# Performance work log

Measured on AMD Instinct MI355X. Metric: run time of the kernel, lower is better.

Reference implementation:

```python
import jax, jax.numpy as jnp
import numpy as np

N, C, H, W = 8, 256, 31, 31
HIDDEN, OUT = 512, 256


def setup_inputs() -> dict:
    key = jax.random.key(0)
    k0, k1, k2, k3, k4 = jax.random.split(key, 5)
    x = jax.random.normal(k0, (N, C, H, W), dtype=jnp.float32)
    # Linear params (torch nn.Linear layout: [out_features, in_features])
    W1 = jax.random.normal(k1, (HIDDEN, C), dtype=jnp.float32) * (1.0 / np.sqrt(C))
    b1 = jax.random.normal(k2, (HIDDEN,), dtype=jnp.float32) * 0.01
    W2 = jax.random.normal(k3, (OUT, HIDDEN), dtype=jnp.float32) * (1.0 / np.sqrt(HIDDEN))
    b2 = jax.random.normal(k4, (OUT,), dtype=jnp.float32) * 0.01
    return {"x": x, "W1": W1, "b1": b1, "W2": W2, "b2": b2}


def _normalized_adjacency(n, h, w):
    M = n * h * w
    idx = jnp.arange(M)
    blk = idx // (h * w)          # sample id of each node
    pos = idx % (h * w)           # spatial position within sample
    # block-diagonal all-ones per sample
    same_block = (blk[:, None] == blk[None, :]).astype(jnp.float32)
    # identity link between consecutive samples (disjoint from block-diag)
    neighbor = ((jnp.abs(blk[:, None] - blk[None, :]) == 1)
                & (pos[:, None] == pos[None, :])).astype(jnp.float32)
    A = same_block + neighbor + jnp.eye(M, dtype=jnp.float32)
    deg = A.sum(axis=1)
    dinv = jnp.where(deg > 0, deg ** -0.5, 0.0)
    return A * dinv[:, None] * dinv[None, :]  # D^-1/2 A D^-1/2


def reference(x, W1, b1, W2, b2):
    n, c, h, w = x.shape
    weight = _normalized_adjacency(n, h, w)                 # [M, M]
    nodes = x.transpose(0, 2, 3, 1).reshape(-1, c)          # [M, C]
    hid = jax.nn.leaky_relu(weight @ nodes @ W1.T + b1)     # [M, HIDDEN]
    hid = jax.nn.leaky_relu(weight @ hid @ W2.T + b2)       # [M, OUT]
    hid = hid.reshape(n, h, w, -1).transpose(0, 3, 1, 2)    # [N, OUT, H, W]
    return hid.max(axis=0, keepdims=True)                   # [1, OUT, H, W]
```

## Files before the change

### kernel.cpp

```cpp
#include <hip/hip_runtime.h>
#include <math.h>

#define NS   8
#define CC   256
#define PP   961
#define MM   7688
#define MP   7744
#define HID  512
#define OUTC 256

typedef _Float16 h16;
using half8   = __attribute__((ext_vector_type(8))) _Float16;
using floatx4 = __attribute__((ext_vector_type(4))) float;

#define AS1 __attribute__((address_space(1)))
#define AS3 __attribute__((address_space(3)))

__device__ __forceinline__ float dinv_of(int b) {
    return (b == 0 || b == NS - 1) ? 0.0322245515f : 0.0322078318f;
}

__global__ void prep(const float* __restrict__ W1, const float* __restrict__ W2,
                     h16* __restrict__ w1h, h16* __restrict__ w2h,
                     const float* __restrict__ x, h16* __restrict__ Xt,
                     float* __restrict__ S1p, float* __restrict__ SY) {
    int blk = blockIdx.x, tid = threadIdx.x;
    if (blk < 256) {
        bool second = blk >= 128;
        const float* src = second ? W2 : W1;
        h16* dst = second ? w2h : w1h;
        int i = ((blk & 127) * 256 + tid) * 4;
        float4 v = *(const float4*)(src + i);
        dst[i + 0] = (h16)v.x; dst[i + 1] = (h16)v.y;
        dst[i + 2] = (h16)v.z; dst[i + 3] = (h16)v.w;
    } else if (blk < 2240) {
        __shared__ h16 tr[32][33];
        int t = blk - 256;
        int b = t & 7, ct = (t >> 3) & 7, pt = t >> 6;
        int p0 = pt * 32, c0 = ct * 32;
        int j = tid & 31, i0 = tid >> 5;
        int p = p0 + j;
        #pragma unroll
        for (int r = 0; r < 4; ++r) {
            int c = c0 + i0 + r * 8;
            float v = (p < PP) ? x[((size_t)b * CC + c) * PP + p] : 0.f;
            tr[i0 + r * 8][j] = (h16)v;
        }
        __syncthreads();
        #pragma unroll
        for (int r = 0; r < 4; ++r) {
            int ii = tid & 31;
            int jj = (tid >> 5) + r * 8;
            int pw = p0 + jj;
            if (pw < PP) {
                int row = ((pw >> 3) << 6) + (b << 3) + (pw & 7);
                Xt[(size_t)row * CC + c0 + ii] = tr[ii][jj];
            }
        }
        if (tid < 32) {
            float s = 0.f;
            #pragma unroll
            for (int jj = 0; jj < 32; ++jj) s += (float)tr[tid][jj];
            S1p[pt * (NS * CC) + b * CC + c0 + tid] = s;
        }
    } else {
        for (int i = tid; i < NS * OUTC; i += 256) SY[i] = 0.f;
    }
}

__global__ void corr(const float* __restrict__ S1p, const float* __restrict__ W1,
                     float* __restrict__ SZc) {
    __shared__ float s1[CC];
    int b = blockIdx.x >> 2, hq = blockIdx.x & 3;
    int tid = threadIdx.x;
    if (tid < CC) {
        float s = 0.f;
        for (int pt = 0; pt < 31; ++pt) s += S1p[pt * (NS * CC) + b * CC + tid];
        s1[tid] = s;
    }
    __syncthreads();
    if (tid < 128) {
        int h = hq * 128 + tid;
        const float* wr = W1 + (size_t)h * CC;
        float dot = 0.f;
        for (int c = 0; c < CC; c += 4) {
            float4 w = *(const float4*)(wr + c);
            dot += s1[c] * w.x + s1[c + 1] * w.y + s1[c + 2] * w.z + s1[c + 3] * w.w;
        }
        float db = dinv_of(b);
        SZc[b * HID + h] = db * db * dot;
    }
}

__global__ __launch_bounds__(256) void gemm1_rho(
    const h16* __restrict__ Xt,
    const h16* __restrict__ B,
    const float* __restrict__ SZc,
    const float* __restrict__ b1v,
    h16* __restrict__ H1)
{
    __shared__ __align__(16) h16 Xs[64 * 64];
    __shared__ __align__(16) h16 Gs[64 * 64];
    __shared__ __align__(16) h16 Bs[64 * 64];
    int tid = threadIdx.x, wave = tid >> 6, lane = tid & 63;
    int rt = blockIdx.x, n0 = blockIdx.y * 64;
    int sro = lane >> 3;
    int sch = (lane & 7) ^ sro;
    const h16* gx0 = Xt + (size_t)(rt * 64 + wave * 16 + sro) * CC + sch * 8;
    const h16* gb0 = B + (size_t)(n0 + wave * 16 + sro) * CC + sch * 8;
    h16* lx0 = &Xs[(wave * 16) * 64];
    h16* lx1 = &Xs[(wave * 16 + 8) * 64];
    h16* lb0 = &Bs[(wave * 16) * 64];
    h16* lb1 = &Bs[(wave * 16 + 8) * 64];
    int fr = lane & 15, fq = lane >> 4;
    int hr = tid >> 2, hc0 = (tid & 3) * 2;
    int hb = hr >> 3;
    float db  = dinv_of(hb);
    float db2 = db * db;
    float dmw = (hb > 0)      ? db * dinv_of(hb - 1) : 0.f;
    float dpw = (hb < NS - 1) ? db * dinv_of(hb + 1) : 0.f;
    int hrm = (hb > 0)      ? hr - 8 : hr;
    int hrp = (hb < NS - 1) ? hr + 8 : hr;
    floatx4 acc[4] = {{0.f,0.f,0.f,0.f},{0.f,0.f,0.f,0.f},{0.f,0.f,0.f,0.f},{0.f,0.f,0.f,0.f}};
    for (int kk = 0; kk < CC; kk += 64) {
        __builtin_amdgcn_global_load_lds((const AS1 void*)(const void*)(gx0 + kk),
                                         (AS3 void*)(void*)lx0, 16, 0, 0);
        __builtin_amdgcn_global_load_lds((const AS1 void*)(const void*)(gx0 + 8 * CC + kk),
                                         (AS3 void*)(void*)lx1, 16, 0, 0);
        __builtin_amdgcn_global_load_lds((const AS1 void*)(const void*)(gb0 + kk),
                                         (AS3 void*)(void*)lb0, 16, 0, 0);
        __builtin_amdgcn_global_load_lds((const AS1 void*)(const void*)(gb0 + 8 * CC + kk),
                                         (AS3 void*)(void*)lb1, 16, 0, 0);
        __syncthreads();
        #pragma unroll
        for (int qi = 0; qi < 2; ++qi) {
            int ch = hc0 + qi;
            int slot = ch ^ (hr & 7);
            half8 zc = *(const half8*)&Xs[hr  * 64 + slot * 8];
            half8 zm = *(const half8*)&Xs[hrm * 64 + slot * 8];
            half8 zp = *(const half8*)&Xs[hrp * 64 + slot * 8];
            half8 o;
            #pragma unroll
            for (int j = 0; j < 8; ++j)
                o[j] = (h16)(db2 * (float)zc[j] + dmw * (float)zm[j] + dpw * (float)zp[j]);
            *(half8*)&Gs[hr * 64 + slot * 8] = o;
        }
        __syncthreads();
        #pragma unroll
        for (int ks = 0; ks < 2; ++ks) {
            int slot = (ks * 4 + fq) ^ (fr & 7);
            half8 bf = *(const half8*)&Bs[(wave * 16 + fr) * 64 + slot * 8];
            #pragma unroll
            for (int mb = 0; mb < 4; ++mb) {
                half8 af = *(const half8*)&Gs[(mb * 16 + fr) * 64 + slot * 8];
                acc[mb] = __builtin_amdgcn_mfma_f32_16x16x32_f16(af, bf, acc[mb], 0, 0, 0);
            }
        }
        __syncthreads();
    }
    int col = n0 + wave * 16 + fr;
    float bv = b1v[col];
    #pragma unroll
    for (int mb = 0; mb < 4; ++mb) {
        #pragma unroll
        for (int r = 0; r < 4; ++r) {
            int row = 16 * mb + 4 * fq + r;
            int b = row >> 3;
            int p = rt * 8 + (row & 7);
            float v = acc[mb][r] + SZc[b * HID + col] + bv;
            v = (v >= 0.f) ? v : 0.01f * v;
            H1[(size_t)(rt * 64 + row) * HID + col] = (p < PP) ? (h16)v : (h16)0.f;
        }
    }
}

__global__ __launch_bounds__(256) void gemm2_sy(
    const h16* __restrict__ A,
    const h16* __restrict__ B,
    float* __restrict__ Y,
    float* __restrict__ SY)
{
    __shared__ __align__(16) h16 As[64 * 64];
    __shared__ __align__(16) h16 Bs[64 * 64];
    int tid = threadIdx.x, wave = tid >> 6, lane = tid & 63;
    int rt = blockIdx.x, n0 = blockIdx.y * 64;
    int sro = lane >> 3;
    int sch = (lane & 7) ^ sro;
    const h16* ga0 = A + (size_t)(rt * 64 + wave * 16 + sro) * HID + sch * 8;
    const h16* gb0 = B + (size_t)(n0 + wave * 16 + sro) * HID + sch * 8;
    h16* la0 = &As[(wave * 16) * 64];
    h16* la1 = &As[(wave * 16 + 8) * 64];
    h16* lb0 = &Bs[(wave * 16) * 64];
    h16* lb1 = &Bs[(wave * 16 + 8) * 64];
    int fr = lane & 15, fq = lane >> 4;
    floatx4 acc[4] = {{0.f,0.f,0.f,0.f},{0.f,0.f,0.f,0.f},{0.f,0.f,0.f,0.f},{0.f,0.f,0.f,0.f}};
    for (int kk = 0; kk < HID; kk += 64) {
        __builtin_amdgcn_global_load_lds((const AS1 void*)(const void*)(ga0 + kk),
                                         (AS3 void*)(void*)la0, 16, 0, 0);
        __builtin_amdgcn_global_load_lds((const AS1 void*)(const void*)(ga0 + 8 * HID + kk),
                                         (AS3 void*)(void*)la1, 16, 0, 0);
        __builtin_amdgcn_global_load_lds((const AS1 void*)(const void*)(gb0 + kk),
                                         (AS3 void*)(void*)lb0, 16, 0, 0);
        __builtin_amdgcn_global_load_lds((const AS1 void*)(const void*)(gb0 + 8 * HID + kk),
                                         (AS3 void*)(void*)lb1, 16, 0, 0);
        __syncthreads();
        #pragma unroll
        for (int ks = 0; ks < 2; ++ks) {
            int slot = (ks * 4 + fq) ^ (fr & 7);
            half8 bf = *(const half8*)&Bs[(wave * 16 + fr) * 64 + slot * 8];
            #pragma unroll
            for (int mb = 0; mb < 4; ++mb) {
                half8 af = *(const half8*)&As[(mb * 16 + fr) * 64 + slot * 8];
                acc[mb] = __builtin_amdgcn_mfma_f32_16x16x32_f16(af, bf, acc[mb], 0, 0, 0);
            }
        }
        __syncthreads();
    }
    int col = n0 + wave * 16 + fr;
    size_t row0 = (size_t)rt * 64;
    float sb[4];
    #pragma unroll
    for (int mb = 0; mb < 4; ++mb) {
        float s = 0.f;
        #pragma unroll
        for (int r = 0; r < 4; ++r) {
            int row = 16 * mb + 4 * fq + r;
            float v = acc[mb][r];
            Y[(row0 + row) * OUTC + col] = v;
            s += v;
        }
        sb[mb] = s;
    }
    #pragma unroll
    for (int mb = 0; mb < 4; ++mb) sb[mb] += __shfl_xor(sb[mb], 16);
    if (fq == 0 || fq == 2) {
        int bodd = (fq >= 2) ? 1 : 0;
        #pragma unroll
        for (int mb = 0; mb < 4; ++mb)
            atomicAdd(&SY[(2 * mb + bodd) * OUTC + col], sb[mb]);
    }
}

__global__ void final_max(const float* __restrict__ Y, const float* __restrict__ SY,
                          const float* __restrict__ b2, float* __restrict__ out) {
    int pt = blockIdx.x, ot = blockIdx.y;
    int p0 = pt * 32, o0 = ot * 32;
    __shared__ float t[32][33];
    int i = threadIdx.x & 31, j0 = threadIdx.x >> 5;
    int o = o0 + i;
    float bias = b2[o];
    #pragma unroll
    for (int r = 0; r < 4; ++r) {
        int j = j0 + r * 8;
        int p = p0 + j;
        float vmax = -INFINITY;
        if (p < PP) {
            size_t rbase = (size_t)(((p >> 3) << 6) + (p & 7)) * OUTC + o;
            float y[NS];
            #pragma unroll
            for (int b = 0; b < NS; ++b)
                y[b] = Y[rbase + (size_t)b * 8 * OUTC];
            #pragma unroll
            for (int b = 0; b < NS; ++b) {
                float db = dinv_of(b);
                float a = db * (SY[b * OUTC + o] + y[b]);
                if (b > 0)      a += dinv_of(b - 1) * y[b - 1];
                if (b < NS - 1) a += dinv_of(b + 1) * y[b + 1];
                float z = db * a + bias;
                z = (z >= 0.f) ? z : 0.01f * z;
                vmax = fmaxf(vmax, z);
            }
        }
        t[j][i] = vmax;
    }
    __syncthreads();
    int jj = threadIdx.x & 31, ii0 = threadIdx.x >> 5;
    #pragma unroll
    for (int r = 0; r < 4; ++r) {
        int ii = ii0 + r * 8;
        int pw = p0 + jj;
        if (pw < PP)
            out[(size_t)(o0 + ii) * PP + pw] = t[jj][ii];
    }
}

extern "C" void kernel_launch(void* const* d_in, const int* in_sizes, int n_in,
                              void* d_out, int out_size, void* d_ws, size_t ws_size,
                              hipStream_t stream) {
    const float* x  = (const float*)d_in[0];
    const float* W1 = (const float*)d_in[1];
    const float* b1 = (const float*)d_in[2];
    const float* W2 = (const float*)d_in[3];
    const float* b2 = (const float*)d_in[4];
    float* out = (float*)d_out;
    float* ws  = (float*)d_ws;

    float* S1p = ws;
    float* SZc = ws + 63488;
    float* SY  = ws + 67584;
    h16*  w1h  = (h16*)(ws + 69632);
    h16*  w2h  = (h16*)(ws + 135168);
    h16*  Xt   = (h16*)(ws + 200704);
    h16*  H1   = (h16*)(ws + 1191936);
    float* Y   = ws + 3174400;

    prep<<<2241, 256, 0, stream>>>(W1, W2, w1h, w2h, x, Xt, S1p, SY);
    corr<<<32, 256, 0, stream>>>(S1p, W1, SZc);
    gemm1_rho<<<dim3(MP / 64, HID / 64), 256, 0, stream>>>(Xt, w1h, SZc, b1, H1);
    gemm2_sy<<<dim3(MP / 64, OUTC / 64), 256, 0, stream>>>(H1, w2h, Y, SY);
    final_max<<<dim3(31, 8), 256, 0, stream>>>(Y, SY, b2, out);
}
```

Measured before the change: 103.5 us.

## Move neighbor mixing into prep and fold per-sample correction rows into gemm1

The inter-sample neighbor mixing (rho) now happens once in prep, written directly as fp16 G, instead of being recomputed per column tile inside gemm1. The per-sample block-sum correction becomes extra rows appended to G, so gemm1 computes it as an extra row tile and the separate corr kernel disappears. The correction add, bias and leaky-relu move into gemm2's A-operand load, which uses register loads instead of direct-to-LDS loads. This removes one launch and the redundant LDS mixing work, but gemm2's A path now pays for extra global loads and ALU work per tile.

New measurement: 99.31 us. 4.1% less time.

```diff
diff --git a/kernel.cpp b/kernel.cpp
--- a/kernel.cpp
+++ b/kernel.cpp
@@ -6,6 +6,7 @@
 #define PP   961
 #define MM   7688
 #define MP   7744
+#define MPX  7808
 #define HID  512
 #define OUTC 256
 
@@ -22,159 +23,135 @@
 
 __global__ void prep(const float* __restrict__ W1, const float* __restrict__ W2,
                      h16* __restrict__ w1h, h16* __restrict__ w2h,
-                     const float* __restrict__ x, h16* __restrict__ Xt,
-                     float* __restrict__ S1p, float* __restrict__ SY) {
+                     const float* __restrict__ x, h16* __restrict__ G,
+                     float* __restrict__ SY) {
     int blk = blockIdx.x, tid = threadIdx.x;
-    if (blk < 256) {
-        bool second = blk >= 128;
+    if (blk < 248) {
+        __shared__ float tr[8][32][33];
+        int pt = blk % 31, ct = blk / 31;
+        int p0 = pt * 32, c0 = ct * 32;
+        int j = tid & 31, i0 = tid >> 5;
+        int p = p0 + j;
+        bool pv = (p < PP);
+        #pragma unroll
+        for (int b = 0; b < NS; ++b)
+            #pragma unroll
+            for (int r = 0; r < 4; ++r) {
+                int c = c0 + i0 + r * 8;
+                tr[b][i0 + r * 8][j] = pv ? x[((size_t)b * CC + c) * PP + p] : 0.f;
+            }
+        __syncthreads();
+        int ii = tid & 31, jj0 = tid >> 5;
+        #pragma unroll
+        for (int b = 0; b < NS; ++b) {
+            float db  = dinv_of(b);
+            float db2 = db * db;
+            float dmw = (b > 0)      ? db * dinv_of(b - 1) : 0.f;
+            float dpw = (b < NS - 1) ? db * dinv_of(b + 1) : 0.f;
+            #pragma unroll
+            for (int r = 0; r < 4; ++r) {
+                int pj = jj0 + r * 8;
+                int pw = p0 + pj;
+                if (pw < 968) {
+                    float v = 0.f;
+                    if (pw < PP) {
+                        v = db2 * tr[b][ii][pj];
+                        if (b > 0)      v += dmw * tr[b - 1][ii][pj];
+                        if (b < NS - 1) v += dpw * tr[b + 1][ii][pj];
+                    }
+                    int row = ((pw >> 3) << 6) + (b << 3) + (pw & 7);
+                    G[(size_t)row * CC + c0 + ii] = (h16)v;
+                }
+            }
+        }
+    } else if (blk < 2296) {
+        int t = blk - 248;
+        int b = t >> 8, c = t & 255;
+        const float* src = x + ((size_t)b * CC + c) * PP;
+        float s = 0.f;
+        for (int i = tid; i < PP; i += 256) s += src[i];
+        __shared__ float red[256];
+        red[tid] = s;
+        __syncthreads();
+        for (int off = 128; off > 0; off >>= 1) {
+            if (tid < off) red[tid] += red[tid + off];
+            __syncthreads();
+        }
+        if (tid == 0) {
+            float db = dinv_of(b);
+            G[(size_t)(MP + b) * CC + c] = (h16)(db * db * red[0]);
+        }
+    } else if (blk < 2552) {
+        int t = blk - 2296;
+        bool second = t >= 128;
         const float* src = second ? W2 : W1;
         h16* dst = second ? w2h : w1h;
-        int i = ((blk & 127) * 256 + tid) * 4;
+        int i = ((t & 127) * 256 + tid) * 4;
         float4 v = *(const float4*)(src + i);
         dst[i + 0] = (h16)v.x; dst[i + 1] = (h16)v.y;
         dst[i + 2] = (h16)v.z; dst[i + 3] = (h16)v.w;
-    } else if (blk < 2240) {
-        __shared__ h16 tr[32][33];
-        int t = blk - 256;
-        int b = t & 7, ct = (t >> 3) & 7, pt = t >> 6;
-        int p0 = pt * 32, c0 = ct * 32;
-        int j = tid & 31, i0 = tid >> 5;
-        int p = p0 + j;
-        #pragma unroll
-        for (int r = 0; r < 4; ++r) {
-            int c = c0 + i0 + r * 8;
-            float v = (p < PP) ? x[((size_t)b * CC + c) * PP + p] : 0.f;
-            tr[i0 + r * 8][j] = (h16)v;
-        }
-        __syncthreads();
-        #pragma unroll
-        for (int r = 0; r < 4; ++r) {
-            int ii = tid & 31;
-            int jj = (tid >> 5) + r * 8;
-            int pw = p0 + jj;
-            if (pw < PP) {
-                int row = ((pw >> 3) << 6) + (b << 3) + (pw & 7);
-                Xt[(size_t)row * CC + c0 + ii] = tr[ii][jj];
-            }
-        }
-        if (tid < 32) {
-            float s = 0.f;
-            #pragma unroll
-            for (int jj = 0; jj < 32; ++jj) s += (float)tr[tid][jj];
-            S1p[pt * (NS * CC) + b * CC + c0 + tid] = s;
-        }
     } else {
         for (int i = tid; i < NS * OUTC; i += 256) SY[i] = 0.f;
-    }
-}
-
-__global__ void corr(const float* __restrict__ S1p, const float* __restrict__ W1,
-                     float* __restrict__ SZc) {
-    __shared__ float s1[CC];
-    int b = blockIdx.x >> 2, hq = blockIdx.x & 3;
-    int tid = threadIdx.x;
-    if (tid < CC) {
-        float s = 0.f;
-        for (int pt = 0; pt < 31; ++pt) s += S1p[pt * (NS * CC) + b * CC + tid];
-        s1[tid] = s;
-    }
-    __syncthreads();
-    if (tid < 128) {
-        int h = hq * 128 + tid;
-        const float* wr = W1 + (size_t)h * CC;
-        float dot = 0.f;
-        for (int c = 0; c < CC; c += 4) {
-            float4 w = *(const float4*)(wr + c);
-            dot += s1[c] * w.x + s1[c + 1] * w.y + s1[c + 2] * w.z + s1[c + 3] * w.w;
-        }
-        float db = dinv_of(b);
-        SZc[b * HID + h] = db * db * dot;
-    }
-}
-
-__global__ __launch_bounds__(256) void gemm1_rho(
-    const h16* __restrict__ Xt,
+        for (int i = tid; i < 56 * CC; i += 256)
+            G[(size_t)(MP + NS) * CC + i] = (h16)0.f;
+    }
+}
+
+__global__ __launch_bounds__(256) void gemm1(
+    const h16* __restrict__ A,
     const h16* __restrict__ B,
-    const float* __restrict__ SZc,
     const float* __restrict__ b1v,
     h16* __restrict__ H1)
 {
-    __shared__ __align__(16) h16 Xs[64 * 64];
-    __shared__ __align__(16) h16 Gs[64 * 64];
+    __shared__ __align__(16) h16 As[64 * 64];
     __shared__ __align__(16) h16 Bs[64 * 64];
     int tid = threadIdx.x, wave = tid >> 6, lane = tid & 63;
     int rt = blockIdx.x, n0 = blockIdx.y * 64;
     int sro = lane >> 3;
     int sch = (lane & 7) ^ sro;
-    const h16* gx0 = Xt + (size_t)(rt * 64 + wave * 16 + sro) * CC + sch * 8;
+    const h16* ga0 = A + (size_t)(rt * 64 + wave * 16 + sro) * CC + sch * 8;
     const h16* gb0 = B + (size_t)(n0 + wave * 16 + sro) * CC + sch * 8;
-    h16* lx0 = &Xs[(wave * 16) * 64];
-    h16* lx1 = &Xs[(wave * 16 + 8) * 64];
+    h16* la0 = &As[(wave * 16) * 64];
+    h16* la1 = &As[(wave * 16 + 8) * 64];
     h16* lb0 = &Bs[(wave * 16) * 64];
     h16* lb1 = &Bs[(wave * 16 + 8) * 64];
     int fr = lane & 15, fq = lane >> 4;
-    int hr = tid >> 2, hc0 = (tid & 3) * 2;
-    int hb = hr >> 3;
-    float db  = dinv_of(hb);
-    float db2 = db * db;
-    float dmw = (hb > 0)      ? db * dinv_of(hb - 1) : 0.f;
-    float dpw = (hb < NS - 1) ? db * dinv_of(hb + 1) : 0.f;
-    int hrm = (hb > 0)      ? hr - 8 : hr;
-    int hrp = (hb < NS - 1) ? hr + 8 : hr;
     floatx4 acc[4] = {{0.f,0.f,0.f,0.f},{0.f,0.f,0.f,0.f},{0.f,0.f,0.f,0.f},{0.f,0.f,0.f,0.f}};
     for (int kk = 0; kk < CC; kk += 64) {
-        __builtin_amdgcn_global_load_lds((const AS1 void*)(const void*)(gx0 + kk),
-                                         (AS3 void*)(void*)lx0, 16, 0, 0);
-        __builtin_amdgcn_global_load_lds((const AS1 void*)(const void*)(gx0 + 8 * CC + kk),
-                                         (AS3 void*)(void*)lx1, 16, 0, 0);
+        __builtin_amdgcn_global_load_lds((const AS1 void*)(const void*)(ga0 + kk),
+                                         (AS3 void*)(void*)la0, 16, 0, 0);
+        __builtin_amdgcn_global_load_lds((const AS1 void*)(const void*)(ga0 + 8 * CC + kk),
+                                         (AS3 void*)(void*)la1, 16, 0, 0);
         __builtin_amdgcn_global_load_lds((const AS1 void*)(const void*)(gb0 + kk),
                                          (AS3 void*)(void*)lb0, 16, 0, 0);
         __builtin_amdgcn_global_load_lds((const AS1 void*)(const void*)(gb0 + 8 * CC + kk),
                                          (AS3 void*)(void*)lb1, 16, 0, 0);
         __syncthreads();
         #pragma unroll
-        for (int qi = 0; qi < 2; ++qi) {
-            int ch = hc0 + qi;
-            int slot = ch ^ (hr & 7);
-            half8 zc = *(const half8*)&Xs[hr  * 64 + slot * 8];
-            half8 zm = *(const half8*)&Xs[hrm * 64 + slot * 8];
-            half8 zp = *(const half8*)&Xs[hrp * 64 + slot * 8];
-            half8 o;
-            #pragma unroll
-            for (int j = 0; j < 8; ++j)
-                o[j] = (h16)(db2 * (float)zc[j] + dmw * (float)zm[j] + dpw * (float)zp[j]);
-            *(half8*)&Gs[hr * 64 + slot * 8] = o;
-        }
-        __syncthreads();
-        #pragma unroll
         for (int ks = 0; ks < 2; ++ks) {
             int slot = (ks * 4 + fq) ^ (fr & 7);
             half8 bf = *(const half8*)&Bs[(wave * 16 + fr) * 64 + slot * 8];
             #pragma unroll
             for (int mb = 0; mb < 4; ++mb) {
-                half8 af = *(const half8*)&Gs[(mb * 16 + fr) * 64 + slot * 8];
+                half8 af = *(const half8*)&As[(mb * 16 + fr) * 64 + slot * 8];
                 acc[mb] = __builtin_amdgcn_mfma_f32_16x16x32_f16(af, bf, acc[mb], 0, 0, 0);
             }
         }
         __syncthreads();
     }
     int col = n0 + wave * 16 + fr;
-    float bv = b1v[col];
-    #pragma unroll
-    for (int mb = 0; mb < 4; ++mb) {
+    float bv = (rt == MP / 64) ? b1v[col] : 0.f;
+    size_t row0 = (size_t)rt * 64;
+    #pragma unroll
+    for (int mb = 0; mb < 4; ++mb)
         #pragma unroll
         for (int r = 0; r < 4; ++r) {
             int row = 16 * mb + 4 * fq + r;
-            int b = row >> 3;
-            int p = rt * 8 + (row & 7);
-            float v = acc[mb][r] + SZc[b * HID + col] + bv;
-            v = (v >= 0.f) ? v : 0.01f * v;
-            H1[(size_t)(rt * 64 + row) * HID + col] = (p < PP) ? (h16)v : (h16)0.f;
-        }
-    }
-}
-
-__global__ __launch_bounds__(256) void gemm2_sy(
+            H1[(row0 + row) * HID + col] = (h16)(acc[mb][r] + bv);
+        }
+}
+
+__global__ __launch_bounds__(256) void gemm2(
     const h16* __restrict__ A,
     const h16* __restrict__ B,
     float* __restrict__ Y,
@@ -185,24 +162,42 @@
     int tid = threadIdx.x, wave = tid >> 6, lane = tid & 63;
     int rt = blockIdx.x, n0 = blockIdx.y * 64;
     int sro = lane >> 3;
-    int sch = (lane & 7) ^ sro;
+    int sch = lane & 7;
+    int schB = sch ^ sro;
     const h16* ga0 = A + (size_t)(rt * 64 + wave * 16 + sro) * HID + sch * 8;
-    const h16* gb0 = B + (size_t)(n0 + wave * 16 + sro) * HID + sch * 8;
-    h16* la0 = &As[(wave * 16) * 64];
-    h16* la1 = &As[(wave * 16 + 8) * 64];
+    const h16* gb0 = B + (size_t)(n0 + wave * 16 + sro) * HID + schB * 8;
+    int b0 = wave * 2;
+    const h16* gt0 = A + (size_t)(MP + b0) * HID + sch * 8;
+    const h16* gt1 = A + (size_t)(MP + b0 + 1) * HID + sch * 8;
+    bool pv = (rt * 8 + sro) < PP;
     h16* lb0 = &Bs[(wave * 16) * 64];
     h16* lb1 = &Bs[(wave * 16 + 8) * 64];
+    int slotA = (sch ^ sro) * 8;
+    h16* lw0 = &As[(wave * 16 + sro) * 64 + slotA];
+    h16* lw1 = &As[(wave * 16 + 8 + sro) * 64 + slotA];
     int fr = lane & 15, fq = lane >> 4;
     floatx4 acc[4] = {{0.f,0.f,0.f,0.f},{0.f,0.f,0.f,0.f},{0.f,0.f,0.f,0.f},{0.f,0.f,0.f,0.f}};
     for (int kk = 0; kk < HID; kk += 64) {
-        __builtin_amdgcn_global_load_lds((const AS1 void*)(const void*)(ga0 + kk),
-                                         (AS3 void*)(void*)la0, 16, 0, 0);
-        __builtin_amdgcn_global_load_lds((const AS1 void*)(const void*)(ga0 + 8 * HID + kk),
-                                         (AS3 void*)(void*)la1, 16, 0, 0);
         __builtin_amdgcn_global_load_lds((const AS1 void*)(const void*)(gb0 + kk),
                                          (AS3 void*)(void*)lb0, 16, 0, 0);
         __builtin_amdgcn_global_load_lds((const AS1 void*)(const void*)(gb0 + 8 * HID + kk),
                                          (AS3 void*)(void*)lb1, 16, 0, 0);
+        half8 a0 = *(const half8*)(ga0 + kk);
+        half8 a1 = *(const half8*)(ga0 + 8 * HID + kk);
+        half8 t0 = *(const half8*)(gt0 + kk);
+        half8 t1 = *(const half8*)(gt1 + kk);
+        half8 o0, o1;
+        #pragma unroll
+        for (int j = 0; j < 8; ++j) {
+            float v0 = (float)a0[j] + (float)t0[j];
+            float v1 = (float)a1[j] + (float)t1[j];
+            v0 = (v0 >= 0.f) ? v0 : 0.01f * v0;
+            v1 = (v1 >= 0.f) ? v1 : 0.01f * v1;
+            o0[j] = pv ? (h16)v0 : (h16)0.f;
+            o1[j] = pv ? (h16)v1 : (h16)0.f;
+        }
+        *(half8*)lw0 = o0;
+        *(half8*)lw1 = o1;
         __syncthreads();
         #pragma unroll
         for (int ks = 0; ks < 2; ++ks) {
@@ -295,18 +290,15 @@
     float* out = (float*)d_out;
     float* ws  = (float*)d_ws;
 
-    float* S1p = ws;
-    float* SZc = ws + 63488;
-    float* SY  = ws + 67584;
-    h16*  w1h  = (h16*)(ws + 69632);
-    h16*  w2h  = (h16*)(ws + 135168);
-    h16*  Xt   = (h16*)(ws + 200704);
-    h16*  H1   = (h16*)(ws + 1191936);
-    float* Y   = ws + 3174400;
-
-    prep<<<2241, 256, 0, stream>>>(W1, W2, w1h, w2h, x, Xt, S1p, SY);
-    corr<<<32, 256, 0, stream>>>(S1p, W1, SZc);
-    gemm1_rho<<<dim3(MP / 64, HID / 64), 256, 0, stream>>>(Xt, w1h, SZc, b1, H1);
-    gemm2_sy<<<dim3(MP / 64, OUTC / 64), 256, 0, stream>>>(H1, w2h, Y, SY);
+    float* SY  = ws;
+    h16*  w1h  = (h16*)(ws + 2048);
+    h16*  w2h  = (h16*)(ws + 67584);
+    h16*  G    = (h16*)(ws + 133120);
+    h16*  H1   = (h16*)(ws + 1132544);
+    float* Y   = ws + 3131392;
+
+    prep<<<2553, 256, 0, stream>>>(W1, W2, w1h, w2h, x, G, SY);
+    gemm1<<<dim3(MPX / 64, HID / 64), 256, 0, stream>>>(G, w1h, b1, H1);
+    gemm2<<<dim3(MP / 64, OUTC / 64), 256, 0, stream>>>(H1, w2h, Y, SY);
     final_max<<<dim3(31, 8), 256, 0, stream>>>(Y, SY, b2, out);
 }
```
